# Performance work log

Measured on AMD Instinct MI355X. Metric: run time of the kernel, lower is better.

Reference implementation:

```python
import jax, jax.numpy as jnp
import numpy as np

D = 256
K = 3  # depthwise conv kernel size (odd)
A_EPS = 1e-4
POW_MIN = 1e-20
LN_EPS = 1e-5


def setup_inputs() -> dict:
    key = jax.random.key(0)
    ks = jax.random.split(key, 10)
    B, H, W = 8, 96, 96
    x = jax.random.normal(ks[0], (B, H, W, D), dtype=jnp.float32)
    inp = {
        'x': x,
        'ln_g': jnp.ones((D,), jnp.float32),
        'ln_b': jnp.zeros((D,), jnp.float32),
        'w_in': jax.random.normal(ks[1], (D, 2 * D), jnp.float32) * 0.02,
        'b_in': jnp.zeros((2 * D,), jnp.float32),
        'conv_w': jax.random.normal(ks[2], (K, K, 1, D), jnp.float32) * 0.1,
        'conv_b': jnp.zeros((D,), jnp.float32),
        'a_logit': 7.0 + 0.1 * jax.random.normal(ks[3], (D,), jnp.float32),
        'ssm_b': jnp.ones((D,), jnp.float32) + 0.02 * jax.random.normal(ks[4], (D,), jnp.float32),
        'ssm_c': jnp.ones((D,), jnp.float32) + 0.02 * jax.random.normal(ks[5], (D,), jnp.float32),
        'ssm_d': jnp.ones((D,), jnp.float32) + 0.02 * jax.random.normal(ks[6], (D,), jnp.float32),
        'w_out': jax.random.normal(ks[7], (D, D), jnp.float32) * 0.02,
        'b_out': jnp.zeros((D,), jnp.float32),
    }
    return inp


def _ssm_scan(x, a_logit, b, c, d):
    # x: (N, L, D). s_t = a*s_{t-1} + b*x_t ; y_t = c*s_t + d*x_t
    # via log-domain cumsum reformulation (as in the torch source).
    L = x.shape[1]
    a = jnp.clip(jax.nn.sigmoid(a_logit), A_EPS, 1.0 - A_EPS)  # (D,)
    t = jnp.arange(L, dtype=jnp.float32)
    a_pow = jnp.maximum(jnp.exp(t[:, None] * jnp.log(a)[None, :]), POW_MIN)  # (L,D)
    u = x * b  # (N,L,D)
    r = jnp.cumsum(u / a_pow[None], axis=1)
    return r * a_pow[None] * c + x * d


def reference(x, ln_g, ln_b, w_in, b_in, conv_w, conv_b,
              a_logit, ssm_b, ssm_c, ssm_d, w_out, b_out):
    B, H, W, Dm = x.shape
    x0 = x
    # LayerNorm over channel dim
    mu = jnp.mean(x, axis=-1, keepdims=True)
    var = jnp.mean(jnp.square(x - mu), axis=-1, keepdims=True)
    h = (x - mu) * jax.lax.rsqrt(var + LN_EPS) * ln_g + ln_b
    # in_proj -> split into value and gate
    xg = h @ w_in + b_in  # (B,H,W,2D)
    x_in, gate = jnp.split(xg, 2, axis=-1)
    gate = jax.nn.sigmoid(gate)
    # depthwise conv (SAME padding) + SiLU, NHWC layout
    u = jax.lax.conv_general_dilated(
        x_in, conv_w, window_strides=(1, 1), padding='SAME',
        dimension_numbers=('NHWC', 'HWIO', 'NHWC'), feature_group_count=Dm)
    u = jax.nn.silu(u + conv_b)
    # 2D bidirectional scan mixing
    L = H * W
    seq_row = u.reshape(B, L, Dm)
    seq_col = u.transpose(0, 2, 1, 3).reshape(B, L, Dm)

    def bid(s):
        yf = _ssm_scan(s, a_logit, ssm_b, ssm_c, ssm_d)
        yb = jnp.flip(_ssm_scan(jnp.flip(s, axis=1), a_logit, ssm_b, ssm_c, ssm_d), axis=1)
        return 0.5 * (yf + yb)

    y_row = bid(seq_row).reshape(B, H, W, Dm)
    y_col = bid(seq_col).reshape(B, W, H, Dm).transpose(0, 2, 1, 3)
    y = 0.5 * (y_row + y_col)
    # gate, out_proj, residual
    y = y * gate
    y = y @ w_out + b_out
    return x0 + y
```

## Files before the change

### kernel.cpp

```cpp
#include <hip/hip_runtime.h>
#include <math.h>

#define DD   256
#define HHH  96
#define WWW  96
#define NB   8
#define LL   9216
#define NPIX (NB*LL)
#define TCH  32
#define NCH  (LL/TCH)

typedef __bf16 bf16_8 __attribute__((ext_vector_type(8)));
typedef float  f32_4  __attribute__((ext_vector_type(4)));

static __device__ __forceinline__ float sigmoidf_(float x) {
    return 1.0f / (1.0f + expf(-x));
}

typedef const __attribute__((address_space(1))) void gas_void;
typedef __attribute__((address_space(3))) void las_void;
static __device__ __forceinline__ void glld16(const void* g, void* l) {
    __builtin_amdgcn_global_load_lds((gas_void*)g, (las_void*)l, 16, 0, 0);
}

template<int DIR>
static __device__ __forceinline__ int spidx(int t) {
    if (DIR == 0) return t;
    int w = t / HHH;
    int h = t - w * HHH;
    return h * WWW + w;
}

__global__ __launch_bounds__(256) void wcvt_kernel(const float* __restrict__ w_in,
                                                   const float* __restrict__ w_out,
                                                   __bf16* __restrict__ w_inT,
                                                   __bf16* __restrict__ w_outT) {
    int i = blockIdx.x * 256 + threadIdx.x;
    int n = i >> 8, k = i & 255;
    w_inT[i] = (__bf16)w_in[k * 512 + n];
    if (i < 256 * 256) w_outT[i] = (__bf16)w_out[k * 256 + n];
}

__global__ __launch_bounds__(256) void ln_kernel(const float* __restrict__ x,
                                                 const float* __restrict__ g,
                                                 const float* __restrict__ b,
                                                 __bf16* __restrict__ h) {
    int wv = threadIdx.x >> 6, lane = threadIdx.x & 63;
    int pix = blockIdx.x * 4 + wv;
    const float4 v = *(const float4*)&x[(size_t)pix * DD + lane * 4];
    float s  = v.x + v.y + v.z + v.w;
    float s2 = v.x * v.x + v.y * v.y + v.z * v.z + v.w * v.w;
    #pragma unroll
    for (int o = 32; o > 0; o >>= 1) {
        s  += __shfl_xor(s, o, 64);
        s2 += __shfl_xor(s2, o, 64);
    }
    float mu  = s * (1.0f / 256.0f);
    float var = s2 * (1.0f / 256.0f) - mu * mu;
    float r = rsqrtf(var + 1e-5f);
    float4 gg = *(const float4*)&g[lane * 4];
    float4 bb = *(const float4*)&b[lane * 4];
    union { ushort4 u; __bf16 e[4]; } o4;
    o4.e[0] = (__bf16)((v.x - mu) * r * gg.x + bb.x);
    o4.e[1] = (__bf16)((v.y - mu) * r * gg.y + bb.y);
    o4.e[2] = (__bf16)((v.z - mu) * r * gg.z + bb.z);
    o4.e[3] = (__bf16)((v.w - mu) * r * gg.w + bb.w);
    *(ushort4*)&h[(size_t)pix * DD + lane * 4] = o4.u;
}

template<int MODE>
__global__ __launch_bounds__(256, 1) void gemm_bf16(const __bf16* __restrict__ A,
                                                 const __bf16* __restrict__ BT,
                                                 const float* __restrict__ bias,
                                                 __bf16* __restrict__ out_xin,
                                                 __bf16* __restrict__ out_gate,
                                                 float* __restrict__ out_f32,
                                                 const float* __restrict__ x0) {
    const int K = 256;
    const int BK = 32;
    __shared__ __bf16 As[8][128 * BK];
    __shared__ __bf16 Bs[8][128 * BK];
    int tid = threadIdx.x;
    int lane = tid & 63, wv = tid >> 6;
    int rowBase = blockIdx.x * 128;
    int colBase = blockIdx.y * 128;

    int srow = tid >> 2, sseg = tid & 3;
    const __bf16* aS0 = A  + (size_t)(rowBase + srow) * K + sseg * 8;
    const __bf16* aS1 = A  + (size_t)(rowBase + srow + 64) * K + sseg * 8;
    const __bf16* bS0 = BT + (size_t)(colBase + srow) * K + sseg * 8;
    const __bf16* bS1 = BT + (size_t)(colBase + srow + 64) * K + sseg * 8;
    int wvoff = wv * 1024;

    int m0 = (wv >> 1) * 64, n0 = (wv & 1) * 64;
    int fr = lane & 15, fq = lane >> 4;
    int rowW = rowBase + m0 + fq * 4;
    int colW = colBase + n0 + fr;

    #pragma unroll
    for (int t = 0; t < 8; ++t) {
        glld16(aS0 + t * BK, (char*)&As[t][0] + wvoff);
        glld16(aS1 + t * BK, (char*)&As[t][0] + 4096 + wvoff);
        glld16(bS0 + t * BK, (char*)&Bs[t][0] + wvoff);
        glld16(bS1 + t * BK, (char*)&Bs[t][0] + 4096 + wvoff);
    }

    float x0r[4][4][4];
    if (MODE == 1) {
        #pragma unroll
        for (int mi = 0; mi < 4; mi++)
            #pragma unroll
            for (int ni = 0; ni < 4; ni++)
                #pragma unroll
                for (int r = 0; r < 4; r++)
                    x0r[mi][ni][r] = x0[(size_t)(rowW + mi * 16 + r) * 256
                                        + colW + ni * 16];
    }

    f32_4 acc[4][4];
    #pragma unroll
    for (int i = 0; i < 4; i++)
        #pragma unroll
        for (int j = 0; j < 4; j++) acc[i][j] = (f32_4){0.f, 0.f, 0.f, 0.f};

    __syncthreads();

    #pragma unroll
    for (int ks = 0; ks < 8; ++ks) {
        bf16_8 af[4], bb[4];
        #pragma unroll
        for (int mi = 0; mi < 4; mi++)
            af[mi] = *(const bf16_8*)&As[ks][(m0 + mi * 16 + fr) * BK + fq * 8];
        #pragma unroll
        for (int ni = 0; ni < 4; ni++)
            bb[ni] = *(const bf16_8*)&Bs[ks][(n0 + ni * 16 + fr) * BK + fq * 8];
        #pragma unroll
        for (int mi = 0; mi < 4; mi++)
            #pragma unroll
            for (int ni = 0; ni < 4; ni++)
                acc[mi][ni] = __builtin_amdgcn_mfma_f32_16x16x32_bf16(
                    af[mi], bb[ni], acc[mi][ni], 0, 0, 0);
    }

    #pragma unroll
    for (int mi = 0; mi < 4; mi++) {
        #pragma unroll
        for (int ni = 0; ni < 4; ni++) {
            int col = colW + ni * 16;
            float bv = bias[col];
            #pragma unroll
            for (int r = 0; r < 4; r++) {
                int row = rowW + mi * 16 + r;
                float v = acc[mi][ni][r] + bv;
                if (MODE == 0) {
                    if (col < 256) {
                        out_xin[(size_t)row * 256 + col] = (__bf16)v;
                    } else {
                        out_gate[(size_t)row * 256 + (col - 256)] = (__bf16)sigmoidf_(v);
                    }
                } else {
                    out_f32[(size_t)row * 256 + col] = v + x0r[mi][ni][r];
                }
            }
        }
    }
}

static __device__ __forceinline__ void loadcol(const __bf16* __restrict__ xin,
                                               int b, int h, int w, int d,
                                               float c[3]) {
    if (w < 0 || w >= WWW) { c[0] = c[1] = c[2] = 0.f; return; }
    size_t base = ((size_t)b * LL + (size_t)h * WWW + w) * DD + d;
    c[0] = (h > 0)       ? (float)xin[base - (size_t)WWW * DD] : 0.f;
    c[1] = (float)xin[base];
    c[2] = (h + 1 < HHH) ? (float)xin[base + (size_t)WWW * DD] : 0.f;
}

__global__ __launch_bounds__(256) void conv_tot_kernel(const __bf16* __restrict__ xin,
                                                       const float* __restrict__ cw,
                                                       const float* __restrict__ cb,
                                                       const float* __restrict__ a_logit,
                                                       const float* __restrict__ ssm_b,
                                                       __bf16* __restrict__ u,
                                                       float* __restrict__ tot_f,
                                                       float* __restrict__ tot_b) {
    int cx = blockIdx.x, h = blockIdx.y, b = blockIdx.z;
    int d = threadIdx.x;
    int w0 = cx * TCH;
    float k[9];
    #pragma unroll
    for (int i = 0; i < 9; i++) k[i] = cw[i * DD + d];
    float bias = cb[d];
    float a = sigmoidf_(a_logit[d]);
    a = fminf(fmaxf(a, 1e-4f), 1.0f - 1e-4f);
    float bb = ssm_b[d];

    float cl[3], cc[3], cr[3];
    loadcol(xin, b, h, w0 - 1, d, cl);
    loadcol(xin, b, h, w0,     d, cc);
    loadcol(xin, b, h, w0 + 1, d, cr);

    float v[TCH];
    float sf = 0.f;
    size_t outBase = ((size_t)b * LL + (size_t)h * WWW + w0) * DD + d;
    #pragma unroll
    for (int j = 0; j < TCH; j++) {
        float nx[3];
        loadcol(xin, b, h, w0 + j + 2, d, nx);
        float acc = bias;
        acc += k[0] * cl[0] + k[1] * cc[0] + k[2] * cr[0];
        acc += k[3] * cl[1] + k[4] * cc[1] + k[5] * cr[1];
        acc += k[6] * cl[2] + k[7] * cc[2] + k[8] * cr[2];
        float uv = acc * sigmoidf_(acc);
        v[j] = uv;
        u[outBase + (size_t)j * DD] = (__bf16)uv;
        sf = a * sf + bb * uv;
        cl[0] = cc[0]; cl[1] = cc[1]; cl[2] = cc[2];
        cc[0] = cr[0]; cc[1] = cr[1]; cc[2] = cr[2];
        cr[0] = nx[0]; cr[1] = nx[1]; cr[2] = nx[2];
    }
    int chunk = h * 3 + cx;
    tot_f[((size_t)b * NCH + chunk) * DD + d] = sf;
    float sb = 0.f;
    #pragma unroll
    for (int j = TCH - 1; j >= 0; j--) sb = a * sb + bb * v[j];
    tot_b[((size_t)b * NCH + chunk) * DD + d] = sb;
}

__global__ __launch_bounds__(256) void scan_totals_col(const __bf16* __restrict__ u,
                                                       const float* __restrict__ a_logit,
                                                       const float* __restrict__ ssm_b,
                                                       float* __restrict__ tot_f,
                                                       float* __restrict__ tot_b) {
    int blk = blockIdx.x;
    int b = blk / NCH, c = blk - b * NCH;
    int d = threadIdx.x;
    float a = sigmoidf_(a_logit[d]);
    a = fminf(fmaxf(a, 1e-4f), 1.0f - 1e-4f);
    float bb = ssm_b[d];
    size_t base = (size_t)b * LL * DD;
    int t0 = c * TCH;
    float v[TCH];
    #pragma unroll
    for (int j = 0; j < TCH; j++)
        v[j] = (float)u[base + (size_t)spidx<1>(t0 + j) * DD + d];
    float s = 0.f;
    #pragma unroll
    for (int j = 0; j < TCH; j++) s = a * s + bb * v[j];
    tot_f[(size_t)blk * DD + d] = s;
    s = 0.f;
    #pragma unroll
    for (int j = TCH - 1; j >= 0; j--) s = a * s + bb * v[j];
    tot_b[(size_t)blk * DD + d] = s;
}

__global__ __launch_bounds__(256) void scan_carries(const float* __restrict__ tot_all,
                                                    const float* __restrict__ a_logit,
                                                    float* __restrict__ car_all) {
    int b = blockIdx.x;
    int var = blockIdx.y;
    int d = threadIdx.x;
    float a = sigmoidf_(a_logit[d]);
    a = fminf(fmaxf(a, 1e-4f), 1.0f - 1e-4f);
    float a2 = a * a, a4 = a2 * a2, a8 = a4 * a4, a16 = a8 * a8;
    float q = a16 * a16;
    const float* tot = tot_all + (size_t)var * NB * NCH * DD + (size_t)b * NCH * DD + d;
    float* car = car_all + (size_t)var * NB * NCH * DD + (size_t)b * NCH * DD + d;
    float P = 0.f;
    if ((var & 1) == 0) {
        for (int c0 = 0; c0 < NCH; c0 += 8) {
            float t[8];
            #pragma unroll
            for (int j = 0; j < 8; j++) t[j] = tot[(size_t)(c0 + j) * DD];
            #pragma unroll
            for (int j = 0; j < 8; j++) {
                car[(size_t)(c0 + j) * DD] = P;
                P = q * P + t[j];
            }
        }
    } else {
        for (int c0 = NCH - 8; c0 >= 0; c0 -= 8) {
            float t[8];
            #pragma unroll
            for (int j = 0; j < 8; j++) t[j] = tot[(size_t)(c0 + j) * DD];
            #pragma unroll
            for (int j = 7; j >= 0; j--) {
                car[(size_t)(c0 + j) * DD] = P;
                P = q * P + t[j];
            }
        }
    }
}

template<int DIR>
__global__ __launch_bounds__(256) void scan_apply(const __bf16* __restrict__ u,
                                                  const float* __restrict__ a_logit,
                                                  const float* __restrict__ ssm_b,
                                                  const float* __restrict__ ssm_c,
                                                  const float* __restrict__ ssm_d,
                                                  const float* __restrict__ car_f,
                                                  const float* __restrict__ car_b,
                                                  float* __restrict__ y,
                                                  const __bf16* __restrict__ gate,
                                                  __bf16* __restrict__ g) {
    int blk = blockIdx.x;
    int b = blk / NCH, c = blk - b * NCH;
    int d = threadIdx.x;
    float a = sigmoidf_(a_logit[d]);
    a = fminf(fmaxf(a, 1e-4f), 1.0f - 1e-4f);
    float bb = ssm_b[d], cc = ssm_c[d], dd = ssm_d[d];
    size_t base = (size_t)b * LL * DD;
    int t0 = c * TCH;
    float v[TCH];
    #pragma unroll
    for (int j = 0; j < TCH; j++)
        v[j] = (float)u[base + (size_t)spidx<DIR>(t0 + j) * DD + d];
    float yf[TCH];
    float s = car_f[(size_t)blk * DD + d];
    #pragma unroll
    for (int j = 0; j < TCH; j++) {
        s = a * s + bb * v[j];
        yf[j] = cc * s + dd * v[j];
    }
    s = car_b[(size_t)blk * DD + d];
    #pragma unroll
    for (int j = TCH - 1; j >= 0; j--) {
        s = a * s + bb * v[j];
        float val = 0.25f * (yf[j] + cc * s + dd * v[j]);
        size_t idx = base + (size_t)spidx<DIR>(t0 + j) * DD + d;
        if (DIR == 0) {
            y[idx] = val;
        } else {
            float t = y[idx] + val;
            g[idx] = (__bf16)(t * (float)gate[idx]);
        }
    }
}

extern "C" void kernel_launch(void* const* d_in, const int* in_sizes, int n_in,
                              void* d_out, int out_size, void* d_ws, size_t ws_size,
                              hipStream_t stream) {
    const float* x       = (const float*)d_in[0];
    const float* ln_g    = (const float*)d_in[1];
    const float* ln_b    = (const float*)d_in[2];
    const float* w_in    = (const float*)d_in[3];
    const float* b_in    = (const float*)d_in[4];
    const float* conv_w  = (const float*)d_in[5];
    const float* conv_b  = (const float*)d_in[6];
    const float* a_logit = (const float*)d_in[7];
    const float* ssm_b   = (const float*)d_in[8];
    const float* ssm_c   = (const float*)d_in[9];
    const float* ssm_d   = (const float*)d_in[10];
    const float* w_out   = (const float*)d_in[11];
    const float* b_out   = (const float*)d_in[12];
    float* out = (float*)d_out;

    char* ws = (char*)d_ws;
    const size_t SZH = (size_t)NPIX * DD * sizeof(__bf16);
    const size_t TS  = (size_t)NB * NCH * DD * sizeof(float);

    __bf16* hB     = (__bf16*)(ws);
    __bf16* xinB   = (__bf16*)(ws + SZH);
    __bf16* uB     = (__bf16*)(ws + 2 * SZH);
    __bf16* gateB  = (__bf16*)(ws + 3 * SZH);
    float*  tot    = (float*)(ws + 4 * SZH);
    float*  car    = (float*)(ws + 4 * SZH + 4 * TS);
    __bf16* w_inT  = (__bf16*)(ws + 4 * SZH + 8 * TS);
    __bf16* w_outT = w_inT + 512 * 256;
    float* y = out;

    wcvt_kernel<<<512, 256, 0, stream>>>(w_in, w_out, w_inT, w_outT);
    ln_kernel<<<NPIX / 4, 256, 0, stream>>>(x, ln_g, ln_b, hB);
    gemm_bf16<0><<<dim3(NPIX / 128, 4), 256, 0, stream>>>(hB, w_inT, b_in,
                                                          xinB, gateB, nullptr, nullptr);
    conv_tot_kernel<<<dim3(WWW / TCH, HHH, NB), 256, 0, stream>>>(
        xinB, conv_w, conv_b, a_logit, ssm_b, uB,
        tot + 0 * (size_t)NB * NCH * DD, tot + 1 * (size_t)NB * NCH * DD);
    scan_totals_col<<<NB * NCH, 256, 0, stream>>>(
        uB, a_logit, ssm_b,
        tot + 2 * (size_t)NB * NCH * DD, tot + 3 * (size_t)NB * NCH * DD);
    scan_carries<<<dim3(NB, 4), 256, 0, stream>>>(tot, a_logit, car);
    scan_apply<0><<<NB * NCH, 256, 0, stream>>>(
        uB, a_logit, ssm_b, ssm_c, ssm_d,
        car + 0 * (size_t)NB * NCH * DD, car + 1 * (size_t)NB * NCH * DD,
        y, nullptr, nullptr);
    scan_apply<1><<<NB * NCH, 256, 0, stream>>>(
        uB, a_logit, ssm_b, ssm_c, ssm_d,
        car + 2 * (size_t)NB * NCH * DD, car + 3 * (size_t)NB * NCH * DD,
        y, gateB, hB);
    gemm_bf16<1><<<dim3(NPIX / 128, 2), 256, 0, stream>>>(hB, w_outT, b_out,
                                                          nullptr, nullptr, out, x);
}
```

Measured before the change: 407.7 us.

## Make GEMMs persistent with LDS-resident weights and register-prefetched A stripes

Both projection GEMMs become persistent kernels. A fixed grid of 128 blocks per column tile loops over 576 row stripes, and each block loads its weight tile into LDS only once. A-operand fragments now come straight from global memory into registers, and the next stripe is prefetched into double-buffered registers (aP/aQ) while the current one runs MFMA. The bias is folded into the accumulator init, and launch bounds are raised to allow two blocks per CU. The cost is heavy register pressure from the prefetch buffers and uncoalesced A loads that skip LDS.

```diff
diff --git a/kernel.cpp b/kernel.cpp
--- a/kernel.cpp
+++ b/kernel.cpp
@@ -9,6 +9,8 @@
 #define NPIX (NB*LL)
 #define TCH  32
 #define NCH  (LL/TCH)
+#define NSTRIPE 576
+#define GXB  128
 
 typedef __bf16 bf16_8 __attribute__((ext_vector_type(8)));
 typedef float  f32_4  __attribute__((ext_vector_type(4)));
@@ -69,7 +71,7 @@
 }
 
 template<int MODE>
-__global__ __launch_bounds__(256, 1) void gemm_bf16(const __bf16* __restrict__ A,
+__global__ __launch_bounds__(256, 2) void gemm_bf16(const __bf16* __restrict__ A,
                                                  const __bf16* __restrict__ BT,
                                                  const float* __restrict__ bias,
                                                  __bf16* __restrict__ out_xin,
@@ -77,93 +79,121 @@
                                                  float* __restrict__ out_f32,
                                                  const float* __restrict__ x0) {
     const int K = 256;
-    const int BK = 32;
-    __shared__ __bf16 As[8][128 * BK];
-    __shared__ __bf16 Bs[8][128 * BK];
+    __shared__ __bf16 Bs[8][128 * 32];
     int tid = threadIdx.x;
     int lane = tid & 63, wv = tid >> 6;
-    int rowBase = blockIdx.x * 128;
     int colBase = blockIdx.y * 128;
 
     int srow = tid >> 2, sseg = tid & 3;
-    const __bf16* aS0 = A  + (size_t)(rowBase + srow) * K + sseg * 8;
-    const __bf16* aS1 = A  + (size_t)(rowBase + srow + 64) * K + sseg * 8;
     const __bf16* bS0 = BT + (size_t)(colBase + srow) * K + sseg * 8;
-    const __bf16* bS1 = BT + (size_t)(colBase + srow + 64) * K + sseg * 8;
+    const __bf16* bS1 = bS0 + (size_t)64 * K;
     int wvoff = wv * 1024;
+    #pragma unroll
+    for (int t = 0; t < 8; ++t) {
+        glld16(bS0 + t * 32, (char*)&Bs[t][0] + wvoff);
+        glld16(bS1 + t * 32, (char*)&Bs[t][0] + 4096 + wvoff);
+    }
 
     int m0 = (wv >> 1) * 64, n0 = (wv & 1) * 64;
     int fr = lane & 15, fq = lane >> 4;
-    int rowW = rowBase + m0 + fq * 4;
-    int colW = colBase + n0 + fr;
-
-    #pragma unroll
-    for (int t = 0; t < 8; ++t) {
-        glld16(aS0 + t * BK, (char*)&As[t][0] + wvoff);
-        glld16(aS1 + t * BK, (char*)&As[t][0] + 4096 + wvoff);
-        glld16(bS0 + t * BK, (char*)&Bs[t][0] + wvoff);
-        glld16(bS1 + t * BK, (char*)&Bs[t][0] + 4096 + wvoff);
-    }
-
-    float x0r[4][4][4];
-    if (MODE == 1) {
+
+    float bv[4];
+    #pragma unroll
+    for (int ni = 0; ni < 4; ni++)
+        bv[ni] = bias[colBase + n0 + ni * 16 + fr];
+
+    const __bf16* Abase = A + (size_t)(m0 + fr) * K + fq * 8;
+
+    bf16_8 aP[4][4], aQ[4][4];
+#define LDA(dst, stripe, half)                                                 \
+    do {                                                                       \
+        const __bf16* p_ = Abase + (size_t)(stripe) * 128 * K + (half) * 128;  \
+        _Pragma("unroll")                                                      \
+        for (int mi_ = 0; mi_ < 4; mi_++)                                      \
+            _Pragma("unroll")                                                  \
+            for (int kk_ = 0; kk_ < 4; kk_++)                                  \
+                dst[mi_][kk_] = *(const bf16_8*)(p_ + (size_t)mi_ * 16 * K     \
+                                                 + kk_ * 32);                  \
+    } while (0)
+
+    int s = blockIdx.x;
+    LDA(aP, s, 0);
+    LDA(aQ, s, 1);
+    __syncthreads();
+
+    while (s < NSTRIPE) {
+        int sn = s + GXB;
+        bool more = (sn < NSTRIPE);
+
+        f32_4 acc[4][4];
         #pragma unroll
         for (int mi = 0; mi < 4; mi++)
             #pragma unroll
             for (int ni = 0; ni < 4; ni++)
+                acc[mi][ni] = (f32_4){bv[ni], bv[ni], bv[ni], bv[ni]};
+
+        #pragma unroll
+        for (int kk = 0; kk < 4; kk++) {
+            bf16_8 bb[4];
+            #pragma unroll
+            for (int ni = 0; ni < 4; ni++)
+                bb[ni] = *(const bf16_8*)&Bs[kk][(n0 + ni * 16 + fr) * 32 + fq * 8];
+            #pragma unroll
+            for (int mi = 0; mi < 4; mi++)
                 #pragma unroll
-                for (int r = 0; r < 4; r++)
-                    x0r[mi][ni][r] = x0[(size_t)(rowW + mi * 16 + r) * 256
-                                        + colW + ni * 16];
-    }
-
-    f32_4 acc[4][4];
-    #pragma unroll
-    for (int i = 0; i < 4; i++)
+                for (int ni = 0; ni < 4; ni++)
+                    acc[mi][ni] = __builtin_amdgcn_mfma_f32_16x16x32_bf16(
+                        aP[mi][kk], bb[ni], acc[mi][ni], 0, 0, 0);
+        }
+        if (more) LDA(aP, sn, 0);
+
         #pragma unroll
-        for (int j = 0; j < 4; j++) acc[i][j] = (f32_4){0.f, 0.f, 0.f, 0.f};
-
-    __syncthreads();
-
-    #pragma unroll
-    for (int ks = 0; ks < 8; ++ks) {
-        bf16_8 af[4], bb[4];
-        #pragma unroll
-        for (int mi = 0; mi < 4; mi++)
-            af[mi] = *(const bf16_8*)&As[ks][(m0 + mi * 16 + fr) * BK + fq * 8];
-        #pragma unroll
-        for (int ni = 0; ni < 4; ni++)
-            bb[ni] = *(const bf16_8*)&Bs[ks][(n0 + ni * 16 + fr) * BK + fq * 8];
-        #pragma unroll
-        for (int mi = 0; mi < 4; mi++)
+        for (int kk = 0; kk < 4; kk++) {
+            bf16_8 bb[4];
             #pragma unroll
             for (int ni = 0; ni < 4; ni++)
-                acc[mi][ni] = __builtin_amdgcn_mfma_f32_16x16x32_bf16(
-                    af[mi], bb[ni], acc[mi][ni], 0, 0, 0);
-    }
-
-    #pragma unroll
-    for (int mi = 0; mi < 4; mi++) {
-        #pragma unroll
-        for (int ni = 0; ni < 4; ni++) {
-            int col = colW + ni * 16;
-            float bv = bias[col];
-            #pragma unroll
-            for (int r = 0; r < 4; r++) {
-                int row = rowW + mi * 16 + r;
-                float v = acc[mi][ni][r] + bv;
-                if (MODE == 0) {
-                    if (col < 256) {
-                        out_xin[(size_t)row * 256 + col] = (__bf16)v;
-                    } else {
-                        out_gate[(size_t)row * 256 + (col - 256)] = (__bf16)sigmoidf_(v);
+                bb[ni] = *(const bf16_8*)&Bs[kk + 4][(n0 + ni * 16 + fr) * 32 + fq * 8];
+            #pragma unroll
+            for (int mi = 0; mi < 4; mi++)
+                #pragma unroll
+                for (int ni = 0; ni < 4; ni++)
+                    acc[mi][ni] = __builtin_amdgcn_mfma_f32_16x16x32_bf16(
+                        aQ[mi][kk], bb[ni], acc[mi][ni], 0, 0, 0);
+        }
+        if (more) LDA(aQ, sn, 1);
+
+        int rowW = s * 128 + m0 + fq * 4;
+        if (MODE == 0) {
+            bool gateBlk = (colBase >= 256);
+            __bf16* outp = gateBlk ? out_gate : out_xin;
+            int colO = colBase + n0 + fr - (gateBlk ? 256 : 0);
+            #pragma unroll
+            for (int mi = 0; mi < 4; mi++)
+                #pragma unroll
+                for (int ni = 0; ni < 4; ni++)
+                    #pragma unroll
+                    for (int r = 0; r < 4; r++) {
+                        float v = acc[mi][ni][r];
+                        if (gateBlk) v = sigmoidf_(v);
+                        outp[(size_t)(rowW + mi * 16 + r) * 256 + colO + ni * 16]
+                            = (__bf16)v;
                     }
-                } else {
-                    out_f32[(size_t)row * 256 + col] = v + x0r[mi][ni][r];
-                }
-            }
-        }
-    }
+        } else {
+            int colW = colBase + n0 + fr;
+            #pragma unroll
+            for (int mi = 0; mi < 4; mi++)
+                #pragma unroll
+                for (int ni = 0; ni < 4; ni++)
+                    #pragma unroll
+                    for (int r = 0; r < 4; r++) {
+                        size_t idx = (size_t)(rowW + mi * 16 + r) * 256
+                                     + colW + ni * 16;
+                        out_f32[idx] = acc[mi][ni][r] + x0[idx];
+                    }
+        }
+        s = sn;
+    }
+#undef LDA
 }
 
 static __device__ __forceinline__ void loadcol(const __bf16* __restrict__ xin,
@@ -371,8 +401,8 @@
 
     wcvt_kernel<<<512, 256, 0, stream>>>(w_in, w_out, w_inT, w_outT);
     ln_kernel<<<NPIX / 4, 256, 0, stream>>>(x, ln_g, ln_b, hB);
-    gemm_bf16<0><<<dim3(NPIX / 128, 4), 256, 0, stream>>>(hB, w_inT, b_in,
-                                                          xinB, gateB, nullptr, nullptr);
+    gemm_bf16<0><<<dim3(GXB, 4), 256, 0, stream>>>(hB, w_inT, b_in,
+                                                   xinB, gateB, nullptr, nullptr);
     conv_tot_kernel<<<dim3(WWW / TCH, HHH, NB), 256, 0, stream>>>(
         xinB, conv_w, conv_b, a_logit, ssm_b, uB,
         tot + 0 * (size_t)NB * NCH * DD, tot + 1 * (size_t)NB * NCH * DD);
@@ -388,6 +418,6 @@
         uB, a_logit, ssm_b, ssm_c, ssm_d,
         car + 2 * (size_t)NB * NCH * DD, car + 3 * (size_t)NB * NCH * DD,
         y, gateB, hB);
-    gemm_bf16<1><<<dim3(NPIX / 128, 2), 256, 0, stream>>>(hB, w_outT, b_out,
-                                                          nullptr, nullptr, out, x);
-}
+    gemm_bf16<1><<<dim3(GXB, 2), 256, 0, stream>>>(hB, w_outT, b_out,
+                                                   nullptr, nullptr, out, x);
+}
```

Result: slower. 549.8 us (+34.9%).
